# Optimization experiments

Measured on AMD Instinct MI355X. Metric: run time of the kernel, lower is better.

Reference implementation:

```python
import jax, jax.numpy as jnp
import numpy as np
from jax import lax


def _sepconv(padded, V, Hk):
    """Per-pixel adaptive separable conv.
    padded: [B,C,H+K-1,W+K-1] (replication-padded frame)
    V, Hk : [B,K,H,W] per-pixel vertical / horizontal 1D kernels
    out[b,c,y,x] = sum_{i,j} padded[b,c,y+i,x+j] * V[b,i,y,x] * Hk[b,j,y,x]
    """
    B, C, Hp, Wp = padded.shape
    K = V.shape[1]
    H, W = Hp - K + 1, Wp - K + 1

    def body(acc, j):
        # columns x+j for all output x: [B,C,Hp,W]
        Pj = lax.dynamic_slice(padded, (0, 0, 0, j), (B, C, Hp, W))
        # vertical windows: [B,C,K,H,W] (K static -> static slices)
        win = jnp.stack([Pj[:, :, i:i + H, :] for i in range(K)], axis=2)
        u = jnp.einsum('bcihw,bihw->bchw', win, V)  # vertical contraction
        acc = acc + u * Hk[:, j][:, None]           # weight by horizontal tap j
        return acc, None

    acc0 = jnp.zeros((B, C, H, W), padded.dtype)
    acc, _ = lax.scan(body, acc0, jnp.arange(K))
    return acc


def setup_inputs() -> dict:
    key = jax.random.key(0)
    ks = jax.random.split(key, 6)
    B, C, H, W, K = 2, 3, 512, 512, 51
    frame0 = jax.random.normal(ks[0], (B, C, H, W), dtype=jnp.float32)
    frame2 = jax.random.normal(ks[1], (B, C, H, W), dtype=jnp.float32)
    V1 = jax.random.uniform(ks[2], (B, K, H, W), dtype=jnp.float32)
    H1 = jax.random.uniform(ks[3], (B, K, H, W), dtype=jnp.float32)
    V2 = jax.random.uniform(ks[4], (B, K, H, W), dtype=jnp.float32)
    H2 = jax.random.uniform(ks[5], (B, K, H, W), dtype=jnp.float32)
    return {"frame0": frame0, "frame2": frame2, "V1": V1, "H1": H1, "V2": V2, "H2": H2}


def reference(frame0, frame2, V1, H1, V2, H2):
    # H=W=512 are multiples of 32, so the %32 zero-padding branch is a no-op.
    K = V1.shape[1]
    p = K // 2  # ReplicationPad2d(kernel_pad)
    rep = lambda x: jnp.pad(x, ((0, 0), (0, 0), (p, p), (p, p)), mode='edge')
    dot1 = _sepconv(rep(frame0), V1, H1)
    dot2 = _sepconv(rep(frame2), V2, H2)
    return dot1 + dot2
```

## Files before the change

### kernel.cpp

```cpp
#include <hip/hip_runtime.h>
#include <stdint.h>

namespace {

typedef _Float16 f16x8 __attribute__((ext_vector_type(8)));
typedef float f32x16 __attribute__((ext_vector_type(16)));

__device__ __forceinline__ uint32_t pkrtz(float a, float b) {
  return __builtin_bit_cast(uint32_t, __builtin_amdgcn_cvt_pkrtz(a, b));
}

constexpr int IMG = 512, K = 51;
constexpr int NT = 512;
constexpr int XB = 64;
constexpr int YB = 8;
constexpr int NSS = YB / 2;
constexpr int FROWS = 59;
constexpr int FG = 15;
constexpr int HP = 26;
constexpr int NQ = 6;

constexpr int GR_B  = FROWS * 16;
constexpr int CH_B  = FG * GR_B;
constexpr int FR_U32 = 3 * FG * FROWS;
constexpr int H_U32  = 2 * 64 * HP;
constexpr int EX_F32 = 4 * 2 * 2 * 2 * 3 * 32;

__device__ __forceinline__ int exidx(int s, int ih, int g, int yp, int c, int n) {
  return ((((s * 2 + ih) * 2 + g) * 2 + yp) * 3 + c) * 32 + n;
}

__global__ __launch_bounds__(NT, 4)
void sepconv(const float* __restrict__ fr0, const float* __restrict__ fr2,
             const float* __restrict__ V1, const float* __restrict__ H1,
             const float* __restrict__ V2, const float* __restrict__ H2,
             float* __restrict__ out)
{
  __shared__ __align__(16) uint32_t fr32[FR_U32 * 4];
  __shared__ uint32_t hL[H_U32];
  __shared__ float exL[EX_F32];

  const int tid = threadIdx.x;
  const int l    = tid & 63;
  const int w    = tid >> 6;
  const int g    = w & 1;
  const int ypar = (w >> 1) & 1;
  const int ih   = w >> 2;
  const int n    = l & 31;
  const int kb   = l >> 5;
  const int x0   = blockIdx.x * XB;
  const int y0   = blockIdx.y * YB;
  const int b    = blockIdx.z;
  const size_t plane = (size_t)IMG * IMG;
  const int xloc = 32 * g + n;

  const int hx = tid & 63, hseg = (tid >> 6) & 3, hyy = tid >> 8;
  const int segp0 = (hseg == 0) ? 0 : (hseg == 1) ? 7 : (hseg == 2) ? 13 : 20;
  const int segn  = (hseg & 1) ? 6 : 7;

  #pragma unroll 1
  for (int f = 0; f < 2; ++f) {
    const float* __restrict__ Vf = (f ? V2 : V1) + (size_t)b * K * plane;
    const float* __restrict__ Hf = (f ? H2 : H1) + (size_t)b * K * plane;
    const float* __restrict__ frb = (f ? fr2 : fr0) + (size_t)b * 3 * plane;

    float ha[7], hb[7];

    __syncthreads();

    float pha[7], phb[7];
    {
      const int yH = y0 + hyy;
      #pragma unroll
      for (int m = 0; m < 7; ++m)
        if (m < segn) {
          int p = segp0 + m, j0 = 2 * p;
          pha[m] = Hf[(size_t)j0 * plane + (size_t)yH * IMG + x0 + hx];
          phb[m] = (j0 + 1 <= 50)
                 ? Hf[(size_t)(j0 + 1) * plane + (size_t)yH * IMG + x0 + hx]
                 : 0.f;
        }
    }
    #pragma unroll 1
    for (int pass = 0; pass < 3; ++pass) {
      float ta[7], tb[7];
      #pragma unroll
      for (int k2 = 0; k2 < 7; ++k2) {
        int task = tid + NT * (pass * 7 + k2);
        if (task < 10620) {
          int rr = task / 180; int rem = task - rr * 180;
          int c = rem / 60, pc = rem - c * 60;
          int row = min(max(y0 - 25 + rr, 0), IMG - 1);
          int ca = min(max(x0 - 25 + 2 * pc, 0), IMG - 1);
          int cb = min(max(x0 - 25 + 2 * pc + 1, 0), IMG - 1);
          const float* rp = frb + (size_t)c * plane + (size_t)row * IMG;
          ta[k2] = rp[ca]; tb[k2] = rp[cb];
        }
      }
      if (pass == 0) {
        #pragma unroll
        for (int m = 0; m < 7; ++m)
          if (m < segn)
            hL[(hyy * 64 + hx) * HP + segp0 + m] = pkrtz(pha[m], phb[m]);
      }
      #pragma unroll
      for (int k2 = 0; k2 < 7; ++k2) {
        int task = tid + NT * (pass * 7 + k2);
        if (task < 10620) {
          int rr = task / 180; int rem = task - rr * 180;
          int c = rem / 60, pc = rem - c * 60;
          fr32[((c * FG + (pc >> 2)) * FROWS + rr) * 4 + (pc & 3)] =
              pkrtz(ta[k2], tb[k2]);
        }
      }
    }
    __syncthreads();

    #pragma unroll 1
    for (int s = 0; s < NSS; ++s) {
      const int y = y0 + 2 * s;
      if (s > 0) {
        __syncthreads();
        #pragma unroll
        for (int m = 0; m < 7; ++m)
          if (m < segn)
            hL[(hyy * 64 + hx) * HP + segp0 + m] = pkrtz(ha[m], hb[m]);
        __syncthreads();
      }
      const int yw = y + ypar;

      const int lr = (ih ? 19 : 0) + 2 * s + ypar + n;
      const char* pA = (const char*)fr32 + (4 * g + kb) * GR_B + lr * 16;
      const uint32_t* hrow = hL + (ypar * 64 + xloc) * HP;
      const bool q5fix = (g & kb) != 0;

      f32x16 D0, D1, D2;
      #pragma unroll
      for (int e = 0; e < 16; ++e) { D0[e] = 0.f; D1[e] = 0.f; D2[e] = 0.f; }

      __builtin_amdgcn_s_setprio(1);
      #pragma unroll 1
      for (int q = 0; q < NQ; ++q) {
        uint4 bq;
        {
          int j0 = 16 * q + 8 * kb - n;
          int pb = j0 >> 1;
          uint32_t rd[5];
          #pragma unroll
          for (int ww = 0; ww < 5; ++ww) {
            int pw = pb + ww;
            bool ok = (unsigned)pw <= 25u;
            uint32_t vr = hrow[ok ? pw : 0];
            rd[ww] = ok ? vr : 0u;
          }
          uint32_t fv[4];
          #pragma unroll
          for (int v2 = 0; v2 < 4; ++v2) {
            uint32_t al =
                (uint32_t)((((uint64_t)rd[v2 + 1] << 32) | rd[v2]) >> 16);
            fv[v2] = (n & 1) ? al : rd[v2];
          }
          bq = make_uint4(fv[0], fv[1], fv[2], fv[3]);
        }
        int aoff = q * (2 * GR_B);
        if (q == 5 && q5fix) aoff -= 2 * GR_B;
        const char* pAq = pA + aoff;
        const f16x8 A0 = *(const f16x8*)(pAq);
        D0 = __builtin_amdgcn_mfma_f32_32x32x16_f16(
                 A0, __builtin_bit_cast(f16x8, bq), D0, 0, 0, 0);
        const f16x8 A1 = *(const f16x8*)(pAq + CH_B);
        D1 = __builtin_amdgcn_mfma_f32_32x32x16_f16(
                 A1, __builtin_bit_cast(f16x8, bq), D1, 0, 0, 0);
        const f16x8 A2 = *(const f16x8*)(pAq + 2 * CH_B);
        D2 = __builtin_amdgcn_mfma_f32_32x32x16_f16(
                 A2, __builtin_bit_cast(f16x8, bq), D2, 0, 0, 0);
      }
      __builtin_amdgcn_s_setprio(0);

      float v[16], vx[3] = {0.f, 0.f, 0.f};
      {
        const float* vb = Vf + (size_t)yw * IMG + x0 + xloc
                          + (size_t)kb * 4 * plane;
        if (ih) {
          const float* vb1 = vb + (size_t)19 * plane;
          #pragma unroll
          for (int r = 0; r < 16; ++r)
            v[r] = vb1[(size_t)((r & 3) + 8 * (r >> 2)) * plane];
        } else {
          #pragma unroll
          for (int r = 0; r < 8; ++r)
            v[r] = vb[(size_t)((r & 3) + 8 * (r >> 2)) * plane];
          if (kb == 0) {
            vx[0] = vb[(size_t)16 * plane];
            vx[1] = vb[(size_t)17 * plane];
            vx[2] = vb[(size_t)18 * plane];
          }
        }
      }
      if (s + 1 < NSS) {
        const int yH = y + 2 + hyy;
        #pragma unroll
        for (int m = 0; m < 7; ++m)
          if (m < segn) {
            int p = segp0 + m, j0 = 2 * p;
            ha[m] = Hf[(size_t)j0 * plane + (size_t)yH * IMG + x0 + hx];
            hb[m] = (j0 + 1 <= 50)
                  ? Hf[(size_t)(j0 + 1) * plane + (size_t)yH * IMG + x0 + hx]
                  : 0.f;
          }
      }

      float a0 = 0.f, a1 = 0.f, a2 = 0.f;
      if (ih) {
        #pragma unroll
        for (int r = 0; r < 16; ++r) {
          a0 += v[r] * D0[r]; a1 += v[r] * D1[r]; a2 += v[r] * D2[r];
        }
      } else {
        #pragma unroll
        for (int r = 0; r < 8; ++r) {
          a0 += v[r] * D0[r]; a1 += v[r] * D1[r]; a2 += v[r] * D2[r];
        }
        a0 += vx[0] * D0[8] + vx[1] * D0[9] + vx[2] * D0[10];
        a1 += vx[0] * D1[8] + vx[1] * D1[9] + vx[2] * D1[10];
        a2 += vx[0] * D2[8] + vx[1] * D2[9] + vx[2] * D2[10];
      }
      a0 += __shfl_xor(a0, 32, 64);
      a1 += __shfl_xor(a1, 32, 64);
      a2 += __shfl_xor(a2, 32, 64);

      if (l < 32) {
        if (f == 0) {
          exL[exidx(s, ih, g, ypar, 0, l)] = a0;
          exL[exidx(s, ih, g, ypar, 1, l)] = a1;
          exL[exidx(s, ih, g, ypar, 2, l)] = a2;
        } else {
          exL[exidx(s, ih, g, ypar, 0, l)] += a0;
          exL[exidx(s, ih, g, ypar, 1, l)] += a1;
          exL[exidx(s, ih, g, ypar, 2, l)] += a2;
        }
      }
    }
  }

  __syncthreads();
  #pragma unroll
  for (int t = 0; t < 3; ++t) {
    int oi = tid + NT * t;
    int px = oi & 63, rem = oi >> 6;
    int c = rem % 3, r = rem / 3;
    int ss = r >> 1, yp = r & 1, gg = px >> 5, nn = px & 31;
    float val = exL[exidx(ss, 0, gg, yp, c, nn)]
              + exL[exidx(ss, 1, gg, yp, c, nn)];
    size_t oidx = ((size_t)(b * 3 + c) * IMG + y0 + r) * IMG + x0 + px;
    out[oidx] = val;
  }
}

}

extern "C" void kernel_launch(void* const* d_in, const int* in_sizes, int n_in,
                              void* d_out, int out_size, void* d_ws, size_t ws_size,
                              hipStream_t stream)
{
  const float* frame0 = (const float*)d_in[0];
  const float* frame2 = (const float*)d_in[1];
  const float* V1 = (const float*)d_in[2];
  const float* H1 = (const float*)d_in[3];
  const float* V2 = (const float*)d_in[4];
  const float* H2 = (const float*)d_in[5];
  float* o = (float*)d_out;

  dim3 grid(IMG / XB, IMG / YB, 2);
  dim3 block(NT);
  hipLaunchKernelGGL(sepconv, grid, block, 0, stream,
                     frame0, frame2, V1, H1, V2, H2, o);
}
```

Baseline: 145.0 us.

## Stage vertical kernels through LDS as fp16 with cooperative prefetch

Replaces per-lane scattered global loads of the V taps after the MFMA loop with a cooperative, pair-coalesced prefetch of the next row pair's V taps into registers. These are written to LDS as packed fp16 alongside the H staging and read back from LDS in the reduction. This hides V load latency behind the MFMA stage and removes the per-thread strided gathers. In exchange it adds LDS footprint and register pressure, which may affect occupancy, and rounds V to fp16, which adds precision error.

New measurement: 288.1 us. 1.99x slower.

```diff
diff --git a/kernel.cpp b/kernel.cpp
--- a/kernel.cpp
+++ b/kernel.cpp
@@ -24,7 +24,9 @@
 constexpr int CH_B  = FG * GR_B;
 constexpr int FR_U32 = 3 * FG * FROWS;
 constexpr int H_U32  = 2 * 64 * HP;
+constexpr int VL_U16 = 2 * 52 * 64;
 constexpr int EX_F32 = 4 * 2 * 2 * 2 * 3 * 32;
+constexpr int NVT = 2 * 51 * 32;
 
 __device__ __forceinline__ int exidx(int s, int ih, int g, int yp, int c, int n) {
   return ((((s * 2 + ih) * 2 + g) * 2 + yp) * 3 + c) * 32 + n;
@@ -38,7 +40,9 @@
 {
   __shared__ __align__(16) uint32_t fr32[FR_U32 * 4];
   __shared__ uint32_t hL[H_U32];
+  __shared__ _Float16 vL[VL_U16];
   __shared__ float exL[EX_F32];
+  uint32_t* vL32 = (uint32_t*)vL;
 
   const int tid = threadIdx.x;
   const int l    = tid & 63;
@@ -65,6 +69,34 @@
     const float* __restrict__ frb = (f ? fr2 : fr0) + (size_t)b * 3 * plane;
 
     float ha[7], hb[7];
+    float vca[7], vcb[7];
+
+    auto loadVC = [&](int yb) {
+      #pragma unroll
+      for (int k = 0; k < 7; ++k) {
+        int t = tid + NT * k;
+        if (t < NVT) {
+          int rowp = (t >= NVT / 2);
+          int rem = t - rowp * (NVT / 2);
+          int tap = rem >> 5, pxp = rem & 31;
+          const float* vp = Vf + ((size_t)tap << 18)
+                            + (size_t)(yb + rowp) * IMG + x0 + 2 * pxp;
+          vca[k] = vp[0]; vcb[k] = vp[1];
+        }
+      }
+    };
+    auto writeVC = [&]() {
+      #pragma unroll
+      for (int k = 0; k < 7; ++k) {
+        int t = tid + NT * k;
+        if (t < NVT) {
+          int rowp = (t >= NVT / 2);
+          int rem = t - rowp * (NVT / 2);
+          int tap = rem >> 5, pxp = rem & 31;
+          vL32[(rowp * 52 + tap) * 32 + pxp] = pkrtz(vca[k], vcb[k]);
+        }
+      }
+    };
 
     __syncthreads();
 
@@ -75,12 +107,13 @@
       for (int m = 0; m < 7; ++m)
         if (m < segn) {
           int p = segp0 + m, j0 = 2 * p;
-          pha[m] = Hf[(size_t)j0 * plane + (size_t)yH * IMG + x0 + hx];
+          pha[m] = Hf[((size_t)j0 << 18) + (size_t)yH * IMG + x0 + hx];
           phb[m] = (j0 + 1 <= 50)
-                 ? Hf[(size_t)(j0 + 1) * plane + (size_t)yH * IMG + x0 + hx]
+                 ? Hf[((size_t)(j0 + 1) << 18) + (size_t)yH * IMG + x0 + hx]
                  : 0.f;
         }
     }
+    loadVC(y0);
     #pragma unroll 1
     for (int pass = 0; pass < 3; ++pass) {
       float ta[7], tb[7];
@@ -103,6 +136,7 @@
           if (m < segn)
             hL[(hyy * 64 + hx) * HP + segp0 + m] = pkrtz(pha[m], phb[m]);
       }
+      if (pass == 1) writeVC();
       #pragma unroll
       for (int k2 = 0; k2 < 7; ++k2) {
         int task = tid + NT * (pass * 7 + k2);
@@ -125,9 +159,9 @@
         for (int m = 0; m < 7; ++m)
           if (m < segn)
             hL[(hyy * 64 + hx) * HP + segp0 + m] = pkrtz(ha[m], hb[m]);
+        writeVC();
         __syncthreads();
       }
-      const int yw = y + ypar;
 
       const int lr = (ih ? 19 : 0) + 2 * s + ypar + n;
       const char* pA = (const char*)fr32 + (4 * g + kb) * GR_B + lr * 16;
@@ -177,53 +211,41 @@
       }
       __builtin_amdgcn_s_setprio(0);
 
-      float v[16], vx[3] = {0.f, 0.f, 0.f};
-      {
-        const float* vb = Vf + (size_t)yw * IMG + x0 + xloc
-                          + (size_t)kb * 4 * plane;
-        if (ih) {
-          const float* vb1 = vb + (size_t)19 * plane;
-          #pragma unroll
-          for (int r = 0; r < 16; ++r)
-            v[r] = vb1[(size_t)((r & 3) + 8 * (r >> 2)) * plane];
-        } else {
-          #pragma unroll
-          for (int r = 0; r < 8; ++r)
-            v[r] = vb[(size_t)((r & 3) + 8 * (r >> 2)) * plane];
-          if (kb == 0) {
-            vx[0] = vb[(size_t)16 * plane];
-            vx[1] = vb[(size_t)17 * plane];
-            vx[2] = vb[(size_t)18 * plane];
-          }
-        }
-      }
       if (s + 1 < NSS) {
         const int yH = y + 2 + hyy;
         #pragma unroll
         for (int m = 0; m < 7; ++m)
           if (m < segn) {
             int p = segp0 + m, j0 = 2 * p;
-            ha[m] = Hf[(size_t)j0 * plane + (size_t)yH * IMG + x0 + hx];
+            ha[m] = Hf[((size_t)j0 << 18) + (size_t)yH * IMG + x0 + hx];
             hb[m] = (j0 + 1 <= 50)
-                  ? Hf[(size_t)(j0 + 1) * plane + (size_t)yH * IMG + x0 + hx]
+                  ? Hf[((size_t)(j0 + 1) << 18) + (size_t)yH * IMG + x0 + hx]
                   : 0.f;
           }
-      }
-
+        loadVC(y + 2);
+      }
+
+      const _Float16* vr0 = vL + (ypar * 52) * 64 + xloc;
       float a0 = 0.f, a1 = 0.f, a2 = 0.f;
       if (ih) {
+        const _Float16* vrb = vr0 + 19 * 64 + kb * 256;
         #pragma unroll
         for (int r = 0; r < 16; ++r) {
-          a0 += v[r] * D0[r]; a1 += v[r] * D1[r]; a2 += v[r] * D2[r];
+          float vt = (float)vrb[((r & 3) + 8 * (r >> 2)) * 64];
+          a0 += vt * D0[r]; a1 += vt * D1[r]; a2 += vt * D2[r];
         }
       } else {
+        const _Float16* vrb = vr0 + kb * 256;
         #pragma unroll
         for (int r = 0; r < 8; ++r) {
-          a0 += v[r] * D0[r]; a1 += v[r] * D1[r]; a2 += v[r] * D2[r];
-        }
-        a0 += vx[0] * D0[8] + vx[1] * D0[9] + vx[2] * D0[10];
-        a1 += vx[0] * D1[8] + vx[1] * D1[9] + vx[2] * D1[10];
-        a2 += vx[0] * D2[8] + vx[1] * D2[9] + vx[2] * D2[10];
+          float vt = (float)vrb[((r & 3) + 8 * (r >> 2)) * 64];
+          a0 += vt * D0[r]; a1 += vt * D1[r]; a2 += vt * D2[r];
+        }
+        #pragma unroll
+        for (int e = 0; e < 3; ++e) {
+          float vt = (kb == 0) ? (float)vr0[(16 + e) * 64] : 0.f;
+          a0 += vt * D0[8 + e]; a1 += vt * D1[8 + e]; a2 += vt * D2[8 + e];
+        }
       }
       a0 += __shfl_xor(a0, 32, 64);
       a1 += __shfl_xor(a1, 32, 64);
```
